# Optimization experiments

Hardware: AMD Instinct MI355X
Metric: run time of the kernel (lower is better)

## Reference

```python
import jax, jax.numpy as jnp
import numpy as np

N_NODES = 100000


def _sage_conv(x, src, dst, W_l, b_l, W_r):
    # PyG SAGEConv (aggr='mean', root_weight=True):
    #   out = lin_l(mean_{j in N(i)} x_j) + lin_r(x_i)
    agg = jax.ops.segment_sum(x[src], dst, num_segments=N_NODES)          # [N, d]
    cnt = jax.ops.segment_sum(jnp.ones(src.shape[0], x.dtype), dst,
                              num_segments=N_NODES)                        # [N]
    mean = agg / jnp.maximum(cnt, 1.0)[:, None]                            # isolated nodes -> 0
    return mean @ W_l + b_l + x @ W_r


def setup_inputs() -> dict:
    key = jax.random.key(0)
    ks = jax.random.split(key, 8)
    dim_in, dim_h, dim_out = 128, 256, 64
    n_edges = 1600000
    x = jax.random.normal(ks[0], (N_NODES, dim_in), dtype=jnp.float32)
    edge_index = jax.random.randint(ks[1], (2, n_edges), 0, N_NODES, dtype=jnp.int32)
    s1 = 1.0 / np.sqrt(dim_in)
    s2 = 1.0 / np.sqrt(dim_h)
    return {
        "x": x,
        "edge_index": edge_index,
        "W1_l": jax.random.uniform(ks[2], (dim_in, dim_h), jnp.float32, -s1, s1),
        "b1": jnp.zeros((dim_h,), jnp.float32),
        "W1_r": jax.random.uniform(ks[3], (dim_in, dim_h), jnp.float32, -s1, s1),
        "W2_l": jax.random.uniform(ks[4], (dim_h, dim_out), jnp.float32, -s2, s2),
        "b2": jnp.zeros((dim_out,), jnp.float32),
        "W2_r": jax.random.uniform(ks[5], (dim_h, dim_out), jnp.float32, -s2, s2),
    }


def reference(x, edge_index, W1_l, b1, W1_r, W2_l, b2, W2_r):
    src, dst = edge_index[0], edge_index[1]
    h = _sage_conv(x, src, dst, W1_l, b1, W1_r)
    h = jax.nn.relu(h)
    # dropout p=0.5 is identity in eval mode (deterministic reference)
    h = _sage_conv(h, src, dst, W2_l, b2, W2_r)
    return jax.nn.log_softmax(h, axis=1)
```

## Files before the change

### kernel.cpp

```cpp
#include <hip/hip_runtime.h>

#define N_NODES 100000
#define N_EDGES 1600000
#define GK 256
#define NBKT 196
#define NBIN 128
#define EPB (N_EDGES / NBIN)

typedef __attribute__((ext_vector_type(8))) short bf16x8;
typedef __attribute__((ext_vector_type(4))) float f32x4;
typedef __attribute__((ext_vector_type(2))) float f32x2;
typedef unsigned short ushort_t;

__device__ __forceinline__ float bf2f(unsigned int bits16) {
  union { unsigned int i; float f; } v; v.i = bits16 << 16; return v.f;
}
__device__ __forceinline__ unsigned short f2bf(float f) {
  union { float f; unsigned int i; } v; v.f = f;
  unsigned int u = v.i;
  unsigned int r = (u + 0x7fffu + ((u >> 16) & 1u)) >> 16;
  return (unsigned short)r;
}
__device__ __forceinline__ unsigned pkbf(f32x2 a) {
  return (unsigned)f2bf(a[0]) | ((unsigned)f2bf(a[1]) << 16);
}
__device__ __forceinline__ void gload16(const void* g, void* l) {
  __builtin_amdgcn_global_load_lds(
      (const __attribute__((address_space(1))) void*)g,
      (__attribute__((address_space(3))) void*)l, 16, 0, 0);
}

#define ACC_U32(u, b) \
  acc[b] += __builtin_amdgcn_cvt_pk_f32_fp8((u), false); \
  acc[(b) + 1] += __builtin_amdgcn_cvt_pk_f32_fp8((u), true);
#define ACC_U4(U, b) \
  ACC_U32((U).x, (b)) ACC_U32((U).y, (b) + 2) ACC_U32((U).z, (b) + 4) ACC_U32((U).w, (b) + 6)


__global__ void zero_int_kernel(int* __restrict__ p, int n) {
  int i = blockIdx.x * blockDim.x + threadIdx.x;
  if (i < n) p[i] = 0;
}

__global__ void bin_count_kernel(const int* __restrict__ dst, int* __restrict__ bucketCount) {
  __shared__ int hist[NBKT];
  int tid = threadIdx.x;
  for (int i = tid; i < NBKT; i += 256) hist[i] = 0;
  __syncthreads();
  const int4* d4 = (const int4*)(dst + blockIdx.x * EPB);
  for (int i = tid; i < EPB / 4; i += 256) {
    int4 v = d4[i];
    atomicAdd(&hist[v.x >> 9], 1); atomicAdd(&hist[v.y >> 9], 1);
    atomicAdd(&hist[v.z >> 9], 1); atomicAdd(&hist[v.w >> 9], 1);
  }
  __syncthreads();
  for (int i = tid; i < NBKT; i += 256)
    if (hist[i]) atomicAdd(&bucketCount[i], hist[i]);
}

__global__ void scan_buckets_kernel(const int* __restrict__ cnt, int* __restrict__ base,
                                    int* __restrict__ cursor, int* __restrict__ rowptr) {
  int lane = threadIdx.x;
  int carry = 0;
  for (int b0 = 0; b0 < NBKT; b0 += 64) {
    int i = b0 + lane;
    int v = (i < NBKT) ? cnt[i] : 0;
    int s = v;
#pragma unroll
    for (int o = 1; o < 64; o <<= 1) { int t = __shfl_up(s, o); if (lane >= o) s += t; }
    int tot = __shfl(s, 63);
    if (i < NBKT) { base[i] = carry + s - v; cursor[i] = carry + s - v; }
    carry += tot;
  }
  if (lane == 0) { base[NBKT] = N_EDGES; rowptr[N_NODES] = N_EDGES; }
}

__global__ void bin_scatter_kernel(const int* __restrict__ src, const int* __restrict__ dst,
                                   int* __restrict__ cursor, unsigned int* __restrict__ pairs) {
  __shared__ int hist[NBKT];
  __shared__ int curs[NBKT];
  int tid = threadIdx.x;
  for (int i = tid; i < NBKT; i += 256) hist[i] = 0;
  __syncthreads();
  const int4* d4 = (const int4*)(dst + blockIdx.x * EPB);
  const int4* s4 = (const int4*)(src + blockIdx.x * EPB);
  for (int i = tid; i < EPB / 4; i += 256) {
    int4 v = d4[i];
    atomicAdd(&hist[v.x >> 9], 1); atomicAdd(&hist[v.y >> 9], 1);
    atomicAdd(&hist[v.z >> 9], 1); atomicAdd(&hist[v.w >> 9], 1);
  }
  __syncthreads();
  for (int i = tid; i < NBKT; i += 256) curs[i] = atomicAdd(&cursor[i], hist[i]);
  __syncthreads();
  for (int i = tid; i < EPB / 4; i += 256) {
    int4 v = d4[i];
    int4 u = s4[i];
    int p;
    p = atomicAdd(&curs[v.x >> 9], 1); pairs[p] = ((unsigned)(v.x & 511) << 17) | (unsigned)u.x;
    p = atomicAdd(&curs[v.y >> 9], 1); pairs[p] = ((unsigned)(v.y & 511) << 17) | (unsigned)u.y;
    p = atomicAdd(&curs[v.z >> 9], 1); pairs[p] = ((unsigned)(v.z & 511) << 17) | (unsigned)u.z;
    p = atomicAdd(&curs[v.w >> 9], 1); pairs[p] = ((unsigned)(v.w & 511) << 17) | (unsigned)u.w;
  }
}

__launch_bounds__(256)
__global__ void bucket_csr_kernel(const unsigned int* __restrict__ pairs,
                                  const int* __restrict__ base,
                                  int* __restrict__ rowptr, int* __restrict__ ebuf) {
  __shared__ int hist[512];
  __shared__ int curs[512];
  __shared__ int wsum[4];
  int b = blockIdx.x;
  int tid = threadIdx.x;
  int n0 = b << 9;
  int nn = N_NODES - n0; if (nn > 512) nn = 512;
  int lo = base[b], hi = base[b + 1];
  hist[tid] = 0; hist[tid + 256] = 0;
  __syncthreads();
  for (int i = lo + tid; i < hi; i += 256)
    atomicAdd(&hist[pairs[i] >> 17], 1);
  __syncthreads();
  int h0 = hist[2 * tid], h1 = hist[2 * tid + 1];
  int ps = h0 + h1;
  int lane = tid & 63, wave = tid >> 6;
  int s = ps;
#pragma unroll
  for (int o = 1; o < 64; o <<= 1) { int t = __shfl_up(s, o); if (lane >= o) s += t; }
  if (lane == 63) wsum[wave] = s;
  __syncthreads();
  if (tid == 0) { int c = 0; for (int k = 0; k < 4; ++k) { int t = wsum[k]; wsum[k] = c; c += t; } }
  __syncthreads();
  int base0 = lo + (s - ps) + wsum[wave];
  curs[2 * tid] = base0;
  curs[2 * tid + 1] = base0 + h0;
  if (2 * tid < nn)     rowptr[n0 + 2 * tid] = base0;
  if (2 * tid + 1 < nn) rowptr[n0 + 2 * tid + 1] = base0 + h0;
  __syncthreads();
  for (int i = lo + tid; i < hi; i += 256) {
    unsigned int p = pairs[i];
    int pos = atomicAdd(&curs[p >> 17], 1);
    ebuf[pos] = (int)(p & 0x1FFFF);
  }
}

#define CVT_X_WORK (N_NODES * 32)
__global__ void cvt_all_kernel(const float* __restrict__ x,
                               const float* __restrict__ W1l, const float* __restrict__ W1r,
                               const float* __restrict__ W2l, const float* __restrict__ W2r,
                               ushort_t* __restrict__ axb, unsigned int* __restrict__ xq,
                               ushort_t* __restrict__ W1bt, ushort_t* __restrict__ W2bt) {
  int idx = blockIdx.x * blockDim.x + threadIdx.x;
  if (idx < CVT_X_WORK) {
    int n = idx >> 5, j = (idx & 31) << 2;
    float4 v = *(const float4*)(x + (size_t)n * 128 + j);
    ushort4 o;
    o.x = f2bf(v.x); o.y = f2bf(v.y); o.z = f2bf(v.z); o.w = f2bf(v.w);
    *(ushort4*)(axb + (size_t)n * 256 + 128 + j) = o;
    unsigned int q = __builtin_amdgcn_cvt_pk_fp8_f32(v.x, v.y, 0, false);
    q = __builtin_amdgcn_cvt_pk_fp8_f32(v.z, v.w, q, true);
    xq[(size_t)n * 32 + (j >> 2)] = q;
  } else if (idx < CVT_X_WORK + 65536) {
    int t = idx - CVT_X_WORK;
    int n = t >> 8, k = t & 255;
    float v = (k < 128) ? W1l[(size_t)k * 256 + n] : W1r[(size_t)(k - 128) * 256 + n];
    W1bt[t] = f2bf(v);
  } else if (idx < CVT_X_WORK + 65536 + 32768) {
    int t = idx - CVT_X_WORK - 65536;
    int n = t >> 8, k = t & 255;
    float v = (n < 64) ? W2l[(size_t)k * 64 + n] : W2r[(size_t)k * 64 + (n - 64)];
    W2bt[t] = f2bf(v);
  }
}

__launch_bounds__(256)
__global__ void agg_mean1_kernel(const int* __restrict__ rowptr, const int* __restrict__ ebuf,
                                 const uint4* __restrict__ xq4, ushort_t* __restrict__ axb) {
  int t = blockIdx.x * 256 + threadIdx.x;
  int node = t >> 3, q = t & 7;
  bool valid = node < N_NODES;
  int anode = valid ? node : 0;
  int beg = rowptr[anode], end = rowptr[anode + 1];
  if (!valid) end = beg;
  f32x2 acc[8];
#pragma unroll
  for (int i = 0; i < 8; ++i) acc[i] = (f32x2){0.f, 0.f};
  int e = beg;
  for (; e + 4 <= end; e += 4) {
    int s0 = ebuf[e], s1 = ebuf[e + 1], s2 = ebuf[e + 2], s3 = ebuf[e + 3];
    uint4 a = xq4[(unsigned)(s0 * 8 + q)];
    uint4 b = xq4[(unsigned)(s1 * 8 + q)];
    uint4 c = xq4[(unsigned)(s2 * 8 + q)];
    uint4 d = xq4[(unsigned)(s3 * 8 + q)];
    ACC_U4(a, 0) ACC_U4(b, 0) ACC_U4(c, 0) ACC_U4(d, 0)
  }
  for (; e < end; ++e) {
    int s = ebuf[e];
    uint4 a = xq4[(unsigned)(s * 8 + q)];
    ACC_U4(a, 0)
  }
  if (!valid) return;
  float inv = (end > beg) ? 1.0f / (float)(end - beg) : 0.0f;
  f32x2 inv2 = {inv, inv};
#pragma unroll
  for (int i = 0; i < 8; ++i) acc[i] *= inv2;
  uint4* orow = (uint4*)(axb + (size_t)node * 256 + q * 16);
  uint4 o0, o1;
  o0.x = pkbf(acc[0]); o0.y = pkbf(acc[1]); o0.z = pkbf(acc[2]); o0.w = pkbf(acc[3]);
  o1.x = pkbf(acc[4]); o1.y = pkbf(acc[5]); o1.z = pkbf(acc[6]); o1.w = pkbf(acc[7]);
  orow[0] = o0;
  orow[1] = o1;
}

template<int MODE>
__launch_bounds__(256)
__global__ void gemm_bf16_kernel(const ushort_t* __restrict__ A, const ushort_t* __restrict__ Bt,
                                 const float* __restrict__ bias, ushort_t* __restrict__ C,
                                 unsigned char* __restrict__ P8, ushort_t* __restrict__ QB,
                                 int M, int NC) {
  __shared__ ushort_t ldsA[128 * 64];
  __shared__ ushort_t ldsB[128 * 64];
  const int tid = threadIdx.x;
  const int lane = tid & 63;
  const int wm = (tid >> 6) & 1, wn = tid >> 7;
  const int rowBase = blockIdx.x * 128;
  const int colBase = blockIdx.y * 128;
  f32x4 acc[4][4];
#pragma unroll
  for (int i = 0; i < 4; ++i)
#pragma unroll
    for (int j = 0; j < 4; ++j) acc[i][j] = (f32x4){0.f, 0.f, 0.f, 0.f};

  for (int k0 = 0; k0 < GK; k0 += 64) {
#pragma unroll
    for (int i = 0; i < 4; ++i) {
      int s = tid + i * 256;
      int row = s >> 3, off16 = s & 7;
      int k16 = off16 ^ (row & 7);
      int ga = rowBase + row; if (ga > M - 1) ga = M - 1;
      gload16(A + (size_t)ga * GK + k0 + k16 * 8, &ldsA[s * 8]);
      gload16(Bt + (size_t)(colBase + row) * GK + k0 + k16 * 8, &ldsB[s * 8]);
    }
    __syncthreads();
#pragma unroll
    for (int kc = 0; kc < 2; ++kc) {
      bf16x8 af[4], bfr[4];
#pragma unroll
      for (int i = 0; i < 4; ++i) {
        int rA = wm * 64 + i * 16 + (lane & 15);
        int oA = (kc * 4 + (lane >> 4)) ^ (rA & 7);
        af[i] = *(const bf16x8*)&ldsA[rA * 64 + oA * 8];
        int rB = wn * 64 + i * 16 + (lane & 15);
        int oB = (kc * 4 + (lane >> 4)) ^ (rB & 7);
        bfr[i] = *(const bf16x8*)&ldsB[rB * 64 + oB * 8];
      }
#pragma unroll
      for (int mi = 0; mi < 4; ++mi)
#pragma unroll
        for (int ni = 0; ni < 4; ++ni)
          acc[mi][ni] = __builtin_amdgcn_mfma_f32_16x16x32_bf16(af[mi], bfr[ni], acc[mi][ni], 0, 0, 0);
    }
    __syncthreads();
  }
#pragma unroll
  for (int mi = 0; mi < 4; ++mi) {
#pragma unroll
    for (int r = 0; r < 4; ++r) {
      int grow = rowBase + wm * 64 + mi * 16 + (lane >> 4) * 4 + r;
      if (grow >= M) continue;
#pragma unroll
      for (int ni = 0; ni < 4; ++ni) {
        float v = acc[mi][ni][r];
        if (MODE == 0) {
          int gcol = colBase + wn * 64 + ni * 16 + (lane & 15);
          C[(size_t)grow * NC + gcol] = f2bf(fmaxf(v + bias[gcol], 0.f));
        } else {
          int c = ni * 16 + (lane & 15);
          if (wn == 0) {
            unsigned int u = __builtin_amdgcn_cvt_pk_fp8_f32(v, v, 0, false);
            P8[(size_t)grow * 64 + c] = (unsigned char)(u & 0xff);
          } else {
            QB[(size_t)grow * 64 + c] = f2bf(v);
          }
        }
      }
    }
  }
}

__launch_bounds__(256)
__global__ void final_kernel(const int* __restrict__ rowptr, const int* __restrict__ ebuf,
                             const uint4* __restrict__ p84, const ushort_t* __restrict__ qb,
                             const float* __restrict__ b2, float* __restrict__ out) {
  int t = blockIdx.x * 256 + threadIdx.x;
  int node = t >> 1, h = t & 1;
  bool valid = node < N_NODES;
  int anode = valid ? node : 0;
  int beg = rowptr[anode], end = rowptr[anode + 1];
  if (!valid) end = beg;
  f32x2 acc[16];
#pragma unroll
  for (int i = 0; i < 16; ++i) acc[i] = (f32x2){0.f, 0.f};
  int e = beg;
  for (; e + 4 <= end; e += 4) {
    int s0 = ebuf[e], s1 = ebuf[e + 1], s2 = ebuf[e + 2], s3 = ebuf[e + 3];
    const uint4* r0 = p84 + (unsigned)(s0 * 4 + h * 2);
    const uint4* r1 = p84 + (unsigned)(s1 * 4 + h * 2);
    const uint4* r2 = p84 + (unsigned)(s2 * 4 + h * 2);
    const uint4* r3 = p84 + (unsigned)(s3 * 4 + h * 2);
    uint4 a0 = r0[0], a1 = r0[1];
    uint4 b0 = r1[0], b1 = r1[1];
    uint4 c0 = r2[0], c1 = r2[1];
    uint4 d0 = r3[0], d1 = r3[1];
    ACC_U4(a0, 0) ACC_U4(a1, 8)
    ACC_U4(b0, 0) ACC_U4(b1, 8)
    ACC_U4(c0, 0) ACC_U4(c1, 8)
    ACC_U4(d0, 0) ACC_U4(d1, 8)
  }
  for (; e < end; ++e) {
    int s = ebuf[e];
    const uint4* rp = p84 + (unsigned)(s * 4 + h * 2);
    uint4 a0 = rp[0], a1 = rp[1];
    ACC_U4(a0, 0) ACC_U4(a1, 8)
  }
  float inv = (end > beg) ? 1.0f / (float)(end - beg) : 0.0f;
  f32x2 inv2 = {inv, inv};
#pragma unroll
  for (int i = 0; i < 16; ++i) acc[i] *= inv2;
  const uint4* qrow = (const uint4*)(qb + (size_t)anode * 64 + h * 32);
  const float* bb = b2 + h * 32;
#pragma unroll
  for (int k = 0; k < 4; ++k) {
    uint4 qv = qrow[k];
    acc[4 * k + 0][0] += bb[8 * k + 0] + bf2f(qv.x & 0xffff);
    acc[4 * k + 0][1] += bb[8 * k + 1] + bf2f(qv.x >> 16);
    acc[4 * k + 1][0] += bb[8 * k + 2] + bf2f(qv.y & 0xffff);
    acc[4 * k + 1][1] += bb[8 * k + 3] + bf2f(qv.y >> 16);
    acc[4 * k + 2][0] += bb[8 * k + 4] + bf2f(qv.z & 0xffff);
    acc[4 * k + 2][1] += bb[8 * k + 5] + bf2f(qv.z >> 16);
    acc[4 * k + 3][0] += bb[8 * k + 6] + bf2f(qv.w & 0xffff);
    acc[4 * k + 3][1] += bb[8 * k + 7] + bf2f(qv.w >> 16);
  }
  float mx[16];
#pragma unroll
  for (int i = 0; i < 16; ++i) mx[i] = fmaxf(acc[i][0], acc[i][1]);
#pragma unroll
  for (int s = 8; s >= 1; s >>= 1)
#pragma unroll
    for (int j = 0; j < 8; ++j)
      if (j < s) mx[j] = fmaxf(mx[j], mx[j + s]);
  float m = fmaxf(mx[0], __shfl_xor(mx[0], 1));
  float sm[16];
#pragma unroll
  for (int i = 0; i < 16; ++i)
    sm[i] = __expf(acc[i][0] - m) + __expf(acc[i][1] - m);
#pragma unroll
  for (int s = 8; s >= 1; s >>= 1)
#pragma unroll
    for (int j = 0; j < 8; ++j)
      if (j < s) sm[j] += sm[j + s];
  float ssum = sm[0] + __shfl_xor(sm[0], 1);
  if (!valid) return;
  float ls = m + __logf(ssum);
  f32x2 ls2 = {ls, ls};
  float4* orow = (float4*)(out + (size_t)node * 64 + h * 32);
#pragma unroll
  for (int i = 0; i < 8; ++i) {
    f32x2 a = acc[2 * i] - ls2;
    f32x2 b = acc[2 * i + 1] - ls2;
    float4 o = {a[0], a[1], b[0], b[1]};
    orow[i] = o;
  }
}


extern "C" void kernel_launch(void* const* d_in, const int* in_sizes, int n_in,
                              void* d_out, int out_size, void* d_ws, size_t ws_size,
                              hipStream_t stream) {
  const float* x   = (const float*)d_in[0];
  const int*   ei  = (const int*)d_in[1];
  const float* W1l = (const float*)d_in[2];
  const float* b1  = (const float*)d_in[3];
  const float* W1r = (const float*)d_in[4];
  const float* W2l = (const float*)d_in[5];
  const float* b2  = (const float*)d_in[6];
  const float* W2r = (const float*)d_in[7];
  float* out = (float*)d_out;
  const int* src = ei;
  const int* dst = ei + N_EDGES;

  char* w = (char*)d_ws;
  int*      bucketCount = (int*)(w);
  int*      bucketBase  = (int*)(w + 1024);
  int*      bucketCur   = (int*)(w + 2048);
  int*      rowptr      = (int*)(w + 4096);
  int*      ebuf        = (int*)(w + 512ull * 1024);
  ushort_t* W1bt        = (ushort_t*)(w + 7ull * 1024 * 1024);
  ushort_t* W2bt        = (ushort_t*)(w + 7ull * 1024 * 1024 + 256 * 1024);
  ushort_t* axb         = (ushort_t*)(w + 8ull * 1024 * 1024);
  ushort_t* h           = (ushort_t*)(w + 60ull * 1024 * 1024);
  unsigned int* pairs   = (unsigned int*)(w + 60ull * 1024 * 1024);
  unsigned int* xq      = (unsigned int*)(w + 112ull * 1024 * 1024);
  unsigned int* p8      = (unsigned int*)(w + 125ull * 1024 * 1024);
  ushort_t*     qb      = (ushort_t*)(w + 132ull * 1024 * 1024);

  zero_int_kernel<<<1, 256, 0, stream>>>(bucketCount, NBKT);
  bin_count_kernel<<<NBIN, 256, 0, stream>>>(dst, bucketCount);
  scan_buckets_kernel<<<1, 64, 0, stream>>>(bucketCount, bucketBase, bucketCur, rowptr);
  bin_scatter_kernel<<<NBIN, 256, 0, stream>>>(src, dst, bucketCur, pairs);
  bucket_csr_kernel<<<NBKT, 256, 0, stream>>>(pairs, bucketBase, rowptr, ebuf);

  const int CVT_TOTAL = CVT_X_WORK + 65536 + 32768;
  cvt_all_kernel<<<(CVT_TOTAL + 255) / 256, 256, 0, stream>>>(
      x, W1l, W1r, W2l, W2r, axb, xq, W1bt, W2bt);

  agg_mean1_kernel<<<(8 * N_NODES + 255) / 256, 256, 0, stream>>>(
      rowptr, ebuf, (const uint4*)xq, axb);

  gemm_bf16_kernel<0><<<dim3((N_NODES + 127) / 128, 2), 256, 0, stream>>>(
      axb, W1bt, b1, h, nullptr, nullptr, N_NODES, 256);
  gemm_bf16_kernel<1><<<dim3((N_NODES + 127) / 128, 1), 256, 0, stream>>>(
      h, W2bt, nullptr, nullptr, (unsigned char*)p8, qb, N_NODES, 128);

  final_kernel<<<(2 * N_NODES + 255) / 256, 256, 0, stream>>>(
      rowptr, ebuf, (const uint4*)p8, qb, b2, out);
}
```

Measured before the change: 195.9 us.

## Fuse histogram with conversion, drop zeroing kernel, widen gather parallelism

Bucket counting and the x/weight conversion now run as one launch. Each bin writes a per-block partial histogram, so the global atomics and the separate zeroing kernel are no longer needed, and a 256-thread scan sums the partials. The layer-1 aggregation loop is unrolled to 8 outstanding gathers per thread. The final kernel uses 4 threads per node instead of 2, each handling 16 columns, with the softmax reduction done over xor shuffles. This trades fewer launches and more memory parallelism for extra scan work and more threads.

```diff
diff --git a/kernel.cpp b/kernel.cpp
--- a/kernel.cpp
+++ b/kernel.cpp
@@ -36,43 +36,72 @@
 #define ACC_U4(U, b) \
   ACC_U32((U).x, (b)) ACC_U32((U).y, (b) + 2) ACC_U32((U).z, (b) + 4) ACC_U32((U).w, (b) + 6)
 
-
-__global__ void zero_int_kernel(int* __restrict__ p, int n) {
-  int i = blockIdx.x * blockDim.x + threadIdx.x;
-  if (i < n) p[i] = 0;
-}
-
-__global__ void bin_count_kernel(const int* __restrict__ dst, int* __restrict__ bucketCount) {
+#define CVT_X_WORK (N_NODES * 32)
+#define CVT_TOTAL (CVT_X_WORK + 65536 + 32768)
+__global__ void count_cvt_kernel(const int* __restrict__ dst, int* __restrict__ partialHist,
+                                 const float* __restrict__ x,
+                                 const float* __restrict__ W1l, const float* __restrict__ W1r,
+                                 const float* __restrict__ W2l, const float* __restrict__ W2r,
+                                 ushort_t* __restrict__ axb, unsigned int* __restrict__ xq,
+                                 ushort_t* __restrict__ W1bt, ushort_t* __restrict__ W2bt) {
   __shared__ int hist[NBKT];
   int tid = threadIdx.x;
-  for (int i = tid; i < NBKT; i += 256) hist[i] = 0;
-  __syncthreads();
-  const int4* d4 = (const int4*)(dst + blockIdx.x * EPB);
-  for (int i = tid; i < EPB / 4; i += 256) {
-    int4 v = d4[i];
-    atomicAdd(&hist[v.x >> 9], 1); atomicAdd(&hist[v.y >> 9], 1);
-    atomicAdd(&hist[v.z >> 9], 1); atomicAdd(&hist[v.w >> 9], 1);
-  }
-  __syncthreads();
-  for (int i = tid; i < NBKT; i += 256)
-    if (hist[i]) atomicAdd(&bucketCount[i], hist[i]);
-}
-
-__global__ void scan_buckets_kernel(const int* __restrict__ cnt, int* __restrict__ base,
+  if (blockIdx.x < NBIN) {
+    for (int i = tid; i < NBKT; i += 256) hist[i] = 0;
+    __syncthreads();
+    const int4* d4 = (const int4*)(dst + blockIdx.x * EPB);
+    for (int i = tid; i < EPB / 4; i += 256) {
+      int4 v = d4[i];
+      atomicAdd(&hist[v.x >> 9], 1); atomicAdd(&hist[v.y >> 9], 1);
+      atomicAdd(&hist[v.z >> 9], 1); atomicAdd(&hist[v.w >> 9], 1);
+    }
+    __syncthreads();
+    for (int i = tid; i < NBKT; i += 256) partialHist[i * NBIN + blockIdx.x] = hist[i];
+  } else {
+    int idx = (blockIdx.x - NBIN) * 256 + tid;
+    if (idx < CVT_X_WORK) {
+      int n = idx >> 5, j = (idx & 31) << 2;
+      float4 v = *(const float4*)(x + (size_t)n * 128 + j);
+      ushort4 o;
+      o.x = f2bf(v.x); o.y = f2bf(v.y); o.z = f2bf(v.z); o.w = f2bf(v.w);
+      *(ushort4*)(axb + (size_t)n * 256 + 128 + j) = o;
+      unsigned int q = __builtin_amdgcn_cvt_pk_fp8_f32(v.x, v.y, 0, false);
+      q = __builtin_amdgcn_cvt_pk_fp8_f32(v.z, v.w, q, true);
+      xq[(size_t)n * 32 + (j >> 2)] = q;
+    } else if (idx < CVT_X_WORK + 65536) {
+      int t = idx - CVT_X_WORK;
+      int n = t >> 8, k = t & 255;
+      float v = (k < 128) ? W1l[(size_t)k * 256 + n] : W1r[(size_t)(k - 128) * 256 + n];
+      W1bt[t] = f2bf(v);
+    } else if (idx < CVT_TOTAL) {
+      int t = idx - CVT_X_WORK - 65536;
+      int n = t >> 8, k = t & 255;
+      float v = (n < 64) ? W2l[(size_t)k * 64 + n] : W2r[(size_t)k * 64 + (n - 64)];
+      W2bt[t] = f2bf(v);
+    }
+  }
+}
+
+__global__ void scan_buckets_kernel(const int* __restrict__ ph, int* __restrict__ base,
                                     int* __restrict__ cursor, int* __restrict__ rowptr) {
-  int lane = threadIdx.x;
-  int carry = 0;
-  for (int b0 = 0; b0 < NBKT; b0 += 64) {
-    int i = b0 + lane;
-    int v = (i < NBKT) ? cnt[i] : 0;
-    int s = v;
-#pragma unroll
-    for (int o = 1; o < 64; o <<= 1) { int t = __shfl_up(s, o); if (lane >= o) s += t; }
-    int tot = __shfl(s, 63);
-    if (i < NBKT) { base[i] = carry + s - v; cursor[i] = carry + s - v; }
-    carry += tot;
-  }
-  if (lane == 0) { base[NBKT] = N_EDGES; rowptr[N_NODES] = N_EDGES; }
+  __shared__ int wsum[4];
+  int t = threadIdx.x;
+  int v = 0;
+  if (t < NBKT) {
+    const int* row = ph + t * NBIN;
+    for (int b = 0; b < NBIN; ++b) v += row[b];
+  }
+  int lane = t & 63, wave = t >> 6;
+  int s = v;
+#pragma unroll
+  for (int o = 1; o < 64; o <<= 1) { int u = __shfl_up(s, o); if (lane >= o) s += u; }
+  if (lane == 63) wsum[wave] = s;
+  __syncthreads();
+  if (t == 0) { int c = 0; for (int k = 0; k < 4; ++k) { int u = wsum[k]; wsum[k] = c; c += u; } }
+  __syncthreads();
+  int excl = s - v + wsum[wave];
+  if (t < NBKT) { base[t] = excl; cursor[t] = excl; }
+  if (t == 0) { base[NBKT] = N_EDGES; rowptr[N_NODES] = N_EDGES; }
 }
 
 __global__ void bin_scatter_kernel(const int* __restrict__ src, const int* __restrict__ dst,
@@ -143,35 +172,6 @@
   }
 }
 
-#define CVT_X_WORK (N_NODES * 32)
-__global__ void cvt_all_kernel(const float* __restrict__ x,
-                               const float* __restrict__ W1l, const float* __restrict__ W1r,
-                               const float* __restrict__ W2l, const float* __restrict__ W2r,
-                               ushort_t* __restrict__ axb, unsigned int* __restrict__ xq,
-                               ushort_t* __restrict__ W1bt, ushort_t* __restrict__ W2bt) {
-  int idx = blockIdx.x * blockDim.x + threadIdx.x;
-  if (idx < CVT_X_WORK) {
-    int n = idx >> 5, j = (idx & 31) << 2;
-    float4 v = *(const float4*)(x + (size_t)n * 128 + j);
-    ushort4 o;
-    o.x = f2bf(v.x); o.y = f2bf(v.y); o.z = f2bf(v.z); o.w = f2bf(v.w);
-    *(ushort4*)(axb + (size_t)n * 256 + 128 + j) = o;
-    unsigned int q = __builtin_amdgcn_cvt_pk_fp8_f32(v.x, v.y, 0, false);
-    q = __builtin_amdgcn_cvt_pk_fp8_f32(v.z, v.w, q, true);
-    xq[(size_t)n * 32 + (j >> 2)] = q;
-  } else if (idx < CVT_X_WORK + 65536) {
-    int t = idx - CVT_X_WORK;
-    int n = t >> 8, k = t & 255;
-    float v = (k < 128) ? W1l[(size_t)k * 256 + n] : W1r[(size_t)(k - 128) * 256 + n];
-    W1bt[t] = f2bf(v);
-  } else if (idx < CVT_X_WORK + 65536 + 32768) {
-    int t = idx - CVT_X_WORK - 65536;
-    int n = t >> 8, k = t & 255;
-    float v = (n < 64) ? W2l[(size_t)k * 64 + n] : W2r[(size_t)k * 64 + (n - 64)];
-    W2bt[t] = f2bf(v);
-  }
-}
-
 __launch_bounds__(256)
 __global__ void agg_mean1_kernel(const int* __restrict__ rowptr, const int* __restrict__ ebuf,
                                  const uint4* __restrict__ xq4, ushort_t* __restrict__ axb) {
@@ -185,13 +185,19 @@
 #pragma unroll
   for (int i = 0; i < 8; ++i) acc[i] = (f32x2){0.f, 0.f};
   int e = beg;
-  for (; e + 4 <= end; e += 4) {
+  for (; e + 8 <= end; e += 8) {
     int s0 = ebuf[e], s1 = ebuf[e + 1], s2 = ebuf[e + 2], s3 = ebuf[e + 3];
+    int s4 = ebuf[e + 4], s5 = ebuf[e + 5], s6 = ebuf[e + 6], s7 = ebuf[e + 7];
     uint4 a = xq4[(unsigned)(s0 * 8 + q)];
     uint4 b = xq4[(unsigned)(s1 * 8 + q)];
     uint4 c = xq4[(unsigned)(s2 * 8 + q)];
     uint4 d = xq4[(unsigned)(s3 * 8 + q)];
+    uint4 f = xq4[(unsigned)(s4 * 8 + q)];
+    uint4 g = xq4[(unsigned)(s5 * 8 + q)];
+    uint4 h2 = xq4[(unsigned)(s6 * 8 + q)];
+    uint4 k = xq4[(unsigned)(s7 * 8 + q)];
     ACC_U4(a, 0) ACC_U4(b, 0) ACC_U4(c, 0) ACC_U4(d, 0)
+    ACC_U4(f, 0) ACC_U4(g, 0) ACC_U4(h2, 0) ACC_U4(k, 0)
   }
   for (; e < end; ++e) {
     int s = ebuf[e];
@@ -292,44 +298,36 @@
                              const uint4* __restrict__ p84, const ushort_t* __restrict__ qb,
                              const float* __restrict__ b2, float* __restrict__ out) {
   int t = blockIdx.x * 256 + threadIdx.x;
-  int node = t >> 1, h = t & 1;
+  int node = t >> 2, q = t & 3;
   bool valid = node < N_NODES;
   int anode = valid ? node : 0;
   int beg = rowptr[anode], end = rowptr[anode + 1];
   if (!valid) end = beg;
-  f32x2 acc[16];
-#pragma unroll
-  for (int i = 0; i < 16; ++i) acc[i] = (f32x2){0.f, 0.f};
+  f32x2 acc[8];
+#pragma unroll
+  for (int i = 0; i < 8; ++i) acc[i] = (f32x2){0.f, 0.f};
   int e = beg;
   for (; e + 4 <= end; e += 4) {
     int s0 = ebuf[e], s1 = ebuf[e + 1], s2 = ebuf[e + 2], s3 = ebuf[e + 3];
-    const uint4* r0 = p84 + (unsigned)(s0 * 4 + h * 2);
-    const uint4* r1 = p84 + (unsigned)(s1 * 4 + h * 2);
-    const uint4* r2 = p84 + (unsigned)(s2 * 4 + h * 2);
-    const uint4* r3 = p84 + (unsigned)(s3 * 4 + h * 2);
-    uint4 a0 = r0[0], a1 = r0[1];
-    uint4 b0 = r1[0], b1 = r1[1];
-    uint4 c0 = r2[0], c1 = r2[1];
-    uint4 d0 = r3[0], d1 = r3[1];
-    ACC_U4(a0, 0) ACC_U4(a1, 8)
-    ACC_U4(b0, 0) ACC_U4(b1, 8)
-    ACC_U4(c0, 0) ACC_U4(c1, 8)
-    ACC_U4(d0, 0) ACC_U4(d1, 8)
+    uint4 a = p84[(unsigned)(s0 * 4 + q)];
+    uint4 b = p84[(unsigned)(s1 * 4 + q)];
+    uint4 c = p84[(unsigned)(s2 * 4 + q)];
+    uint4 d = p84[(unsigned)(s3 * 4 + q)];
+    ACC_U4(a, 0) ACC_U4(b, 0) ACC_U4(c, 0) ACC_U4(d, 0)
   }
   for (; e < end; ++e) {
     int s = ebuf[e];
-    const uint4* rp = p84 + (unsigned)(s * 4 + h * 2);
-    uint4 a0 = rp[0], a1 = rp[1];
-    ACC_U4(a0, 0) ACC_U4(a1, 8)
+    uint4 a = p84[(unsigned)(s * 4 + q)];
+    ACC_U4(a, 0)
   }
   float inv = (end > beg) ? 1.0f / (float)(end - beg) : 0.0f;
   f32x2 inv2 = {inv, inv};
 #pragma unroll
-  for (int i = 0; i < 16; ++i) acc[i] *= inv2;
-  const uint4* qrow = (const uint4*)(qb + (size_t)anode * 64 + h * 32);
-  const float* bb = b2 + h * 32;
-#pragma unroll
-  for (int k = 0; k < 4; ++k) {
+  for (int i = 0; i < 8; ++i) acc[i] *= inv2;
+  const uint4* qrow = (const uint4*)(qb + (size_t)anode * 64 + q * 16);
+  const float* bb = b2 + q * 16;
+#pragma unroll
+  for (int k = 0; k < 2; ++k) {
     uint4 qv = qrow[k];
     acc[4 * k + 0][0] += bb[8 * k + 0] + bf2f(qv.x & 0xffff);
     acc[4 * k + 0][1] += bb[8 * k + 1] + bf2f(qv.x >> 16);
@@ -340,31 +338,35 @@
     acc[4 * k + 3][0] += bb[8 * k + 6] + bf2f(qv.w & 0xffff);
     acc[4 * k + 3][1] += bb[8 * k + 7] + bf2f(qv.w >> 16);
   }
-  float mx[16];
-#pragma unroll
-  for (int i = 0; i < 16; ++i) mx[i] = fmaxf(acc[i][0], acc[i][1]);
-#pragma unroll
-  for (int s = 8; s >= 1; s >>= 1)
-#pragma unroll
-    for (int j = 0; j < 8; ++j)
+  float mx[8];
+#pragma unroll
+  for (int i = 0; i < 8; ++i) mx[i] = fmaxf(acc[i][0], acc[i][1]);
+#pragma unroll
+  for (int s = 4; s >= 1; s >>= 1)
+#pragma unroll
+    for (int j = 0; j < 4; ++j)
       if (j < s) mx[j] = fmaxf(mx[j], mx[j + s]);
-  float m = fmaxf(mx[0], __shfl_xor(mx[0], 1));
-  float sm[16];
-#pragma unroll
-  for (int i = 0; i < 16; ++i)
+  float m = mx[0];
+  m = fmaxf(m, __shfl_xor(m, 1));
+  m = fmaxf(m, __shfl_xor(m, 2));
+  float sm[8];
+#pragma unroll
+  for (int i = 0; i < 8; ++i)
     sm[i] = __expf(acc[i][0] - m) + __expf(acc[i][1] - m);
 #pragma unroll
-  for (int s = 8; s >= 1; s >>= 1)
-#pragma unroll
-    for (int j = 0; j < 8; ++j)
+  for (int s = 4; s >= 1; s >>= 1)
+#pragma unroll
+    for (int j = 0; j < 4; ++j)
       if (j < s) sm[j] += sm[j + s];
-  float ssum = sm[0] + __shfl_xor(sm[0], 1);
+  float ssum = sm[0];
+  ssum += __shfl_xor(ssum, 1);
+  ssum += __shfl_xor(ssum, 2);
   if (!valid) return;
   float ls = m + __logf(ssum);
   f32x2 ls2 = {ls, ls};
-  float4* orow = (float4*)(out + (size_t)node * 64 + h * 32);
-#pragma unroll
-  for (int i = 0; i < 8; ++i) {
+  float4* orow = (float4*)(out + (size_t)node * 64 + q * 16);
+#pragma unroll
+  for (int i = 0; i < 4; ++i) {
     f32x2 a = acc[2 * i] - ls2;
     f32x2 b = acc[2 * i + 1] - ls2;
     float4 o = {a[0], a[1], b[0], b[1]};
@@ -389,29 +391,26 @@
   const int* dst = ei + N_EDGES;
 
   char* w = (char*)d_ws;
-  int*      bucketCount = (int*)(w);
-  int*      bucketBase  = (int*)(w + 1024);
-  int*      bucketCur   = (int*)(w + 2048);
-  int*      rowptr      = (int*)(w + 4096);
-  int*      ebuf        = (int*)(w + 512ull * 1024);
-  ushort_t* W1bt        = (ushort_t*)(w + 7ull * 1024 * 1024);
-  ushort_t* W2bt        = (ushort_t*)(w + 7ull * 1024 * 1024 + 256 * 1024);
-  ushort_t* axb         = (ushort_t*)(w + 8ull * 1024 * 1024);
-  ushort_t* h           = (ushort_t*)(w + 60ull * 1024 * 1024);
-  unsigned int* pairs   = (unsigned int*)(w + 60ull * 1024 * 1024);
-  unsigned int* xq      = (unsigned int*)(w + 112ull * 1024 * 1024);
-  unsigned int* p8      = (unsigned int*)(w + 125ull * 1024 * 1024);
-  ushort_t*     qb      = (ushort_t*)(w + 132ull * 1024 * 1024);
-
-  zero_int_kernel<<<1, 256, 0, stream>>>(bucketCount, NBKT);
-  bin_count_kernel<<<NBIN, 256, 0, stream>>>(dst, bucketCount);
-  scan_buckets_kernel<<<1, 64, 0, stream>>>(bucketCount, bucketBase, bucketCur, rowptr);
+  int*      bucketBase  = (int*)(w);
+  int*      bucketCur   = (int*)(w + 1024);
+  int*      partialHist = (int*)(w + 2048);
+  int*      rowptr      = (int*)(w + 128ull * 1024);
+  int*      ebuf        = (int*)(w + 1024ull * 1024);
+  ushort_t* W1bt        = (ushort_t*)(w + 8ull * 1024 * 1024);
+  ushort_t* W2bt        = (ushort_t*)(w + 8ull * 1024 * 1024 + 256 * 1024);
+  ushort_t* axb         = (ushort_t*)(w + 9ull * 1024 * 1024);
+  ushort_t* h           = (ushort_t*)(w + 61ull * 1024 * 1024);
+  unsigned int* pairs   = (unsigned int*)(w + 61ull * 1024 * 1024);
+  unsigned int* xq      = (unsigned int*)(w + 113ull * 1024 * 1024);
+  unsigned int* p8      = (unsigned int*)(w + 126ull * 1024 * 1024);
+  ushort_t*     qb      = (ushort_t*)(w + 133ull * 1024 * 1024);
+
+  const int CVT_BLOCKS = (CVT_TOTAL + 255) / 256;
+  count_cvt_kernel<<<NBIN + CVT_BLOCKS, 256, 0, stream>>>(
+      dst, partialHist, x, W1l, W1r, W2l, W2r, axb, xq, W1bt, W2bt);
+  scan_buckets_kernel<<<1, 256, 0, stream>>>(partialHist, bucketBase, bucketCur, rowptr);
   bin_scatter_kernel<<<NBIN, 256, 0, stream>>>(src, dst, bucketCur, pairs);
   bucket_csr_kernel<<<NBKT, 256, 0, stream>>>(pairs, bucketBase, rowptr, ebuf);
-
-  const int CVT_TOTAL = CVT_X_WORK + 65536 + 32768;
-  cvt_all_kernel<<<(CVT_TOTAL + 255) / 256, 256, 0, stream>>>(
-      x, W1l, W1r, W2l, W2r, axb, xq, W1bt, W2bt);
 
   agg_mean1_kernel<<<(8 * N_NODES + 255) / 256, 256, 0, stream>>>(
       rowptr, ebuf, (const uint4*)xq, axb);
@@ -421,6 +420,6 @@
   gemm_bf16_kernel<1><<<dim3((N_NODES + 127) / 128, 1), 256, 0, stream>>>(
       h, W2bt, nullptr, nullptr, (unsigned char*)p8, qb, N_NODES, 128);
 
-  final_kernel<<<(2 * N_NODES + 255) / 256, 256, 0, stream>>>(
+  final_kernel<<<(4 * N_NODES + 255) / 256, 256, 0, stream>>>(
       rowptr, ebuf, (const uint4*)p8, qb, b2, out);
 }
```

After: 186.9 us. 4.6% less time.
